# Kernel optimization log

Hardware: AMD Instinct MI355X
Metric: run time of the kernel (lower is better)

The kernel has to match this reference:

```python
import jax, jax.numpy as jnp
import numpy as np

H_HEADS = 32
KV_HEADS = 8
HEAD_DIM = 128
HIDDEN = 2048
EPS = 1e-6


def rms_norm(x, w):
    # normalize over last dim (head_dim)
    var = jnp.mean(jnp.square(x), axis=-1, keepdims=True)
    return x * jax.lax.rsqrt(var + EPS) * w


def rotate_half(x):
    x1, x2 = jnp.split(x, 2, axis=-1)
    return jnp.concatenate([-x2, x1], axis=-1)


def setup_inputs() -> dict:
    key = jax.random.key(0)
    ks = jax.random.split(key, 8)
    B, Q, CTX = 1, 1024, 2048
    T = CTX + Q
    hidden_states = jax.random.normal(ks[0], (B, Q, HIDDEN), jnp.float32)
    target_hidden = jax.random.normal(ks[1], (B, CTX, HIDDEN), jnp.float32)
    # RoPE tables over the full concatenated length
    inv_freq = 1.0 / (10000.0 ** (np.arange(0, HEAD_DIM, 2, dtype=np.float32) / HEAD_DIM))
    pos = np.arange(T, dtype=np.float32)
    freqs = np.outer(pos, inv_freq)                     # [T, hd/2]
    emb = np.concatenate([freqs, freqs], axis=-1)       # [T, hd]
    cos = jnp.asarray(np.cos(emb))[None]                # [1, T, hd]
    sin = jnp.asarray(np.sin(emb))[None]
    # custom mask: context fully visible, causal within noise block
    noise_causal = jnp.tril(jnp.ones((Q, Q), bool))
    mask = jnp.concatenate([jnp.ones((Q, CTX), bool), noise_causal], axis=1)
    attention_mask = mask[None, None]                   # [1,1,Q,T]
    scale = 0.02
    wq = jax.random.normal(ks[2], (H_HEADS * HEAD_DIM, HIDDEN), jnp.float32) * scale
    wk = jax.random.normal(ks[3], (KV_HEADS * HEAD_DIM, HIDDEN), jnp.float32) * scale
    wv = jax.random.normal(ks[4], (KV_HEADS * HEAD_DIM, HIDDEN), jnp.float32) * scale
    wo = jax.random.normal(ks[5], (HIDDEN, H_HEADS * HEAD_DIM), jnp.float32) * scale
    q_norm_w = jnp.ones((HEAD_DIM,), jnp.float32)
    k_norm_w = jnp.ones((HEAD_DIM,), jnp.float32)
    return {"hidden_states": hidden_states, "target_hidden": target_hidden,
            "cos": cos, "sin": sin, "attention_mask": attention_mask,
            "wq": wq, "wk": wk, "wv": wv, "wo": wo,
            "q_norm_w": q_norm_w, "k_norm_w": k_norm_w}


def reference(hidden_states, target_hidden, cos, sin, attention_mask,
              wq, wk, wv, wo, q_norm_w, k_norm_w):
    B, Q, _ = hidden_states.shape
    CTX = target_hidden.shape[1]
    T = CTX + Q
    n_rep = H_HEADS // KV_HEADS
    scaling = HEAD_DIM ** -0.5

    # Q from noise tokens, QK-RMSNorm per head
    q = (hidden_states @ wq.T).reshape(B, Q, H_HEADS, HEAD_DIM)
    q = rms_norm(q, q_norm_w).transpose(0, 2, 1, 3)          # [B,H,Q,hd]

    # K/V: context then noise, concatenated along sequence
    k = jnp.concatenate([target_hidden @ wk.T, hidden_states @ wk.T], axis=1)
    k = rms_norm(k.reshape(B, T, KV_HEADS, HEAD_DIM), k_norm_w).transpose(0, 2, 1, 3)  # [B,Hk,T,hd]
    v = jnp.concatenate([target_hidden @ wv.T, hidden_states @ wv.T], axis=1)
    v = v.reshape(B, T, KV_HEADS, HEAD_DIM).transpose(0, 2, 1, 3)                       # [B,Hk,T,hd]

    # offset RoPE: K uses all T positions, Q uses the last Q positions
    cos_b = cos[:, None]                                      # [B,1,T,hd]
    sin_b = sin[:, None]
    q = q * cos_b[:, :, -Q:, :] + rotate_half(q) * sin_b[:, :, -Q:, :]
    k = k * cos_b + rotate_half(k) * sin_b

    # GQA attention without materializing repeated K/V
    qg = q.reshape(B, KV_HEADS, n_rep, Q, HEAD_DIM)
    scores = jnp.einsum('bgrqd,bgtd->bgrqt', qg, k) * scaling  # [B,Hk,rep,Q,T]
    scores = jnp.where(attention_mask[:, :, None], scores, jnp.finfo(scores.dtype).min)
    probs = jax.nn.softmax(scores, axis=-1)
    out = jnp.einsum('bgrqt,bgtd->bgrqd', probs, v)            # [B,Hk,rep,Q,hd]
    out = out.reshape(B, H_HEADS, Q, HEAD_DIM).transpose(0, 2, 1, 3).reshape(B, Q, H_HEADS * HEAD_DIM)
    return out @ wo.T
```

## Files before the change

### kernel.cpp

```cpp
#include <hip/hip_runtime.h>

#define HIDDEN 2048
#define NQ     1024
#define NCTX   2048
#define NTOT   3072
#define NHEADS 32
#define KVH    8
#define HD     128

typedef __attribute__((ext_vector_type(8))) __bf16 bf16x8;
typedef __attribute__((ext_vector_type(4))) __bf16 bf16x4;
typedef __attribute__((ext_vector_type(4))) float  f32x4;

#define MFMA16(a, b, c) __builtin_amdgcn_mfma_f32_16x16x32_bf16(a, b, c, 0, 0, 0)

#define MSTATIC 12.0f

__device__ __forceinline__ void load_lds16(const void* g, void* l) {
    __builtin_amdgcn_global_load_lds(
        (const __attribute__((address_space(1))) unsigned int*)g,
        (__attribute__((address_space(3))) unsigned int*)l, 16, 0, 0);
}

__global__ __launch_bounds__(256) void conv2_f32_bf16(const float* __restrict__ s0,
                                                      __bf16* __restrict__ d0, int n0,
                                                      const float* __restrict__ s1,
                                                      __bf16* __restrict__ d1, int n1) {
    const float* s = blockIdx.y ? s1 : s0;
    __bf16*      d = blockIdx.y ? d1 : d0;
    int          n = blockIdx.y ? n1 : n0;
    int i = blockIdx.x * 256 + threadIdx.x;
    int stride = gridDim.x * 256;
    for (; i < n; i += stride) {
        float4 v = ((const float4*)s)[i];
        bf16x4 o;
        o[0] = (__bf16)v.x; o[1] = (__bf16)v.y;
        o[2] = (__bf16)v.z; o[3] = (__bf16)v.w;
        ((bf16x4*)d)[i] = o;
    }
}

template <typename OutT>
__device__ __forceinline__ void gemm128_f32b(const __bf16* __restrict__ Ablk,
                                             const float* __restrict__ Bblk,
                                             OutT* __restrict__ Cblk,
                                             int K, int lda, int ldb, int ldc) {
    __shared__ __bf16 As[128][64];
    __shared__ __bf16 Bs[128][64];

    const int tid  = threadIdx.x;
    const int lane = tid & 63;
    const int w    = tid >> 6;
    const int n16  = lane & 15;
    const int quad = lane >> 4;
    const int wm = (w & 1) * 64;
    const int wn = (w >> 1) * 64;

    f32x4 acc[4][4];
    const f32x4 fzero = {0.f, 0.f, 0.f, 0.f};
#pragma unroll
    for (int i = 0; i < 4; i++)
#pragma unroll
        for (int j = 0; j < 4; j++) acc[i][j] = fzero;

    const int srow = w * 32 + (lane >> 3);
    const int scol = (lane & 7) * 8;

    for (int k0 = 0; k0 < K; k0 += 64) {
#pragma unroll
        for (int i = 0; i < 4; i++) {
            int r = srow + i * 8;
            load_lds16(Ablk + (long)r * lda + k0 + scol, &As[r][scol]);
        }
#pragma unroll
        for (int i = 0; i < 4; i++) {
            int id = tid + i * 256;
            int br = id >> 3, c8 = (id & 7) * 8;
            float4 f0 = *(const float4*)(Bblk + (long)br * ldb + k0 + c8);
            float4 f1 = *(const float4*)(Bblk + (long)br * ldb + k0 + c8 + 4);
            bf16x8 bb;
            bb[0] = (__bf16)f0.x; bb[1] = (__bf16)f0.y;
            bb[2] = (__bf16)f0.z; bb[3] = (__bf16)f0.w;
            bb[4] = (__bf16)f1.x; bb[5] = (__bf16)f1.y;
            bb[6] = (__bf16)f1.z; bb[7] = (__bf16)f1.w;
            *(bf16x8*)&Bs[br][c8] = bb;
        }
        __syncthreads();
#pragma unroll
        for (int ks = 0; ks < 2; ks++) {
            bf16x8 af[4], bfr[4];
#pragma unroll
            for (int i = 0; i < 4; i++)
                af[i] = *(const bf16x8*)&As[wm + i * 16 + n16][ks * 32 + quad * 8];
#pragma unroll
            for (int j = 0; j < 4; j++)
                bfr[j] = *(const bf16x8*)&Bs[wn + j * 16 + n16][ks * 32 + quad * 8];
#pragma unroll
            for (int i = 0; i < 4; i++)
#pragma unroll
                for (int j = 0; j < 4; j++)
                    acc[i][j] = MFMA16(af[i], bfr[j], acc[i][j]);
        }
        __syncthreads();
    }

#pragma unroll
    for (int i = 0; i < 4; i++)
#pragma unroll
        for (int j = 0; j < 4; j++)
#pragma unroll
            for (int r = 0; r < 4; r++)
                Cblk[(long)(wm + i * 16 + quad * 4 + r) * ldc + wn + j * 16 + n16] =
                    (OutT)acc[i][j][r];
}

__global__ __launch_bounds__(256) void gemm_kvq(const __bf16* __restrict__ tgtb,
                                                const __bf16* __restrict__ hidb,
                                                const float* __restrict__ wk,
                                                const float* __restrict__ wv,
                                                const float* __restrict__ wq,
                                                __bf16* __restrict__ kbf,
                                                __bf16* __restrict__ vbf,
                                                __bf16* __restrict__ qbf) {
    const int b = blockIdx.x;
    const __bf16* Ap; const float* Bp; __bf16* Cp; int ldc;
    if (b < 384) {
        const int z = b / 192, bb = b - z * 192;
        const int n0 = (bb & 7) * 128, m0 = (bb >> 3) * 128;
        Ap = (m0 < 2048) ? tgtb + (long)m0 * 2048 : hidb + (long)(m0 - 2048) * 2048;
        Bp = (z ? wv : wk) + (long)n0 * 2048;
        Cp = (z ? vbf : kbf) + (long)m0 * 1024 + n0;
        ldc = 1024;
    } else {
        const int bb = b - 384;
        const int n0 = (bb & 31) * 128, m0 = (bb >> 5) * 128;
        Ap = hidb + (long)m0 * 2048;
        Bp = wq + (long)n0 * 2048;
        Cp = qbf + (long)m0 * 4096 + n0;
        ldc = 4096;
    }
    gemm128_f32b<__bf16>(Ap, Bp, Cp, 2048, 2048, 2048, ldc);
}

__global__ __launch_bounds__(256) void gemm_wo_splitk(const __bf16* __restrict__ A,
                                                      const float* __restrict__ B,
                                                      float* __restrict__ po) {
    const int m0 = blockIdx.y * 128;
    const int n0 = blockIdx.x * 128;
    const int koff = blockIdx.z * 1024;
    float* C = po + (long)blockIdx.z * 1024 * 2048;
    gemm128_f32b<float>(A + (long)m0 * 4096 + koff, B + (long)n0 * 4096 + koff,
                        C + (long)m0 * 2048 + n0, 1024, 4096, 4096, 2048);
}

__global__ __launch_bounds__(256) void add4(const float* __restrict__ po,
                                            float* __restrict__ out, int n4) {
    int i = blockIdx.x * 256 + threadIdx.x;
    int stride = gridDim.x * 256;
    const long seg = (long)1024 * 2048 / 4;
    for (; i < n4; i += stride) {
        float4 a = ((const float4*)po)[i];
        float4 b = ((const float4*)po)[i + seg];
        float4 c = ((const float4*)po)[i + 2 * seg];
        float4 d = ((const float4*)po)[i + 3 * seg];
        float4 o;
        o.x = (a.x + b.x) + (c.x + d.x);
        o.y = (a.y + b.y) + (c.y + d.y);
        o.z = (a.z + b.z) + (c.z + d.z);
        o.w = (a.w + b.w) + (c.w + d.w);
        ((float4*)out)[i] = o;
    }
}

__global__ __launch_bounds__(256) void rmsnorm_rope2(__bf16* __restrict__ xq,
                                                     const float* __restrict__ wq,
                                                     __bf16* __restrict__ xk,
                                                     const float* __restrict__ wk,
                                                     const float* __restrict__ cosb,
                                                     const float* __restrict__ sinb) {
    const int z = blockIdx.y;
    __bf16*      x = z ? xk : xq;
    const float* w = z ? wk : wq;
    const int nheads     = z ? 8 : 32;
    const int row_stride = z ? 1024 : 4096;
    const int pos_offset = z ? 0 : 2048;
    const float outscale = z ? 1.0f : 0.08838834764831845f;
    const int nitems     = z ? 3072 * 8 : 1024 * 32;

    int item = blockIdx.x * 4 + (threadIdx.x >> 6);
    int lane = threadIdx.x & 63;
    if (item >= nitems) return;
    int row = item / nheads;
    int head = item - row * nheads;
    __bf16* p = x + (long)row * row_stride + head * HD;

    float x1 = (float)p[lane], x2 = (float)p[lane + 64];
    float ss = x1 * x1 + x2 * x2;
#pragma unroll
    for (int o = 32; o >= 1; o >>= 1) ss += __shfl_xor(ss, o);
    float r = rsqrtf(ss * (1.0f / 128.0f) + 1e-6f) * outscale;

    int pos = pos_offset + row;
    float c1 = cosb[pos * HD + lane], c2 = cosb[pos * HD + lane + 64];
    float s1 = sinb[pos * HD + lane], s2 = sinb[pos * HD + lane + 64];
    float y1 = x1 * r * w[lane];
    float y2 = x2 * r * w[lane + 64];
    p[lane]      = (__bf16)(y1 * c1 - y2 * s1);
    p[lane + 64] = (__bf16)(y2 * c2 + y1 * s2);
}

__global__ __launch_bounds__(256) void transpose_v(const __bf16* __restrict__ v,
                                                   __bf16* __restrict__ vt) {
    __shared__ __bf16 T[64][68];
    const int tid = threadIdx.x;
    const int t0 = blockIdx.x * 64;
    const int d0 = blockIdx.y * 64;
    const int g  = blockIdx.z;
    const __bf16* src = v + (long)t0 * 1024 + g * 128 + d0;
#pragma unroll
    for (int i = 0; i < 4; i++) {
        int idx = tid + i * 256;
        int r = idx >> 4, c4 = (idx & 15) * 4;
        *(bf16x4*)&T[r][c4] = *(const bf16x4*)(src + (long)r * 1024 + c4);
    }
    __syncthreads();
    __bf16* dst = vt + (long)g * 128 * 3072 + (long)d0 * 3072 + t0;
#pragma unroll
    for (int i = 0; i < 4; i++) {
        int idx = tid + i * 256;
        int r = idx >> 4, c4 = (idx & 15) * 4;
        bf16x4 o;
        o[0] = T[c4 + 0][r]; o[1] = T[c4 + 1][r];
        o[2] = T[c4 + 2][r]; o[3] = T[c4 + 3][r];
        *(bf16x4*)(dst + (long)r * 3072 + c4) = o;
    }
}

__global__ __launch_bounds__(256) void flash_attn_splitk(const __bf16* __restrict__ qb,
                                                         const __bf16* __restrict__ kb,
                                                         const __bf16* __restrict__ vtg,
                                                         __bf16* __restrict__ Opart0,
                                                         __bf16* __restrict__ Opart1,
                                                         float* __restrict__ lsum) {
    __shared__ __bf16 KsU[64 * 136];
    __shared__ __bf16 Vs[128][72];
#define KS(r, c) KsU[(r) * 136 + (c)]
#define PS(w_, m_, t_) KsU[(w_) * 2176 + (m_) * 68 + (t_)]

    const int tid  = threadIdx.x;
    const int lane = tid & 63;
    const int w    = tid >> 6;
    const int n    = lane & 15;
    const int quad = lane >> 4;

    const int bid = blockIdx.x;
    const int s   = blockIdx.y;
    const int g  = bid & 7;
    const int jj = bid >> 3;
    const int h  = g * 4 + (jj & 3);
    const int qt = jj >> 2;

    const int qr0 = qt * 128 + w * 16;

    bf16x8 qf[2][4];
#pragma unroll
    for (int mt = 0; mt < 2; mt++) {
        const __bf16* qp = qb + (long)(qr0 + mt * 64 + n) * 4096 + h * 128 + quad * 8;
        qf[mt][0] = *(const bf16x8*)(qp);
        qf[mt][1] = *(const bf16x8*)(qp + 32);
        qf[mt][2] = *(const bf16x8*)(qp + 64);
        qf[mt][3] = *(const bf16x8*)(qp + 96);
    }

    f32x4 O[2][8];
    const f32x4 fzero = {0.f, 0.f, 0.f, 0.f};
#pragma unroll
    for (int mt = 0; mt < 2; mt++)
#pragma unroll
        for (int dt = 0; dt < 8; dt++) O[mt][dt] = fzero;
    float l_loc[2] = {0.f, 0.f};

    const int ntot = 34 + 2 * qt;
    const int half = ntot >> 1;
    const int tbeg = s ? half : 0;
    const int tend = s ? ntot : half;

    const int krr = tid >> 4, kc8 = (tid & 15) * 8;
    const int vrr = tid >> 3, vc8 = (tid & 7) * 8;
    const __bf16* kp = kb + g * 128 + (long)(tbeg * 64 + krr) * 1024 + kc8;
    const __bf16* vp = vtg + (long)g * 128 * 3072 + (long)vrr * 3072 + tbeg * 64 + vc8;

    for (int tt = tbeg; tt < tend; tt++) {
#pragma unroll
        for (int i = 0; i < 4; i++)
            *(bf16x8*)&KS(krr + i * 16, kc8) = *(const bf16x8*)(kp + (long)i * 16 * 1024);
#pragma unroll
        for (int i = 0; i < 4; i++)
            *(bf16x8*)&Vs[vrr + i * 32][vc8] = *(const bf16x8*)(vp + (long)i * 32 * 3072);
        kp += 64 * 1024;
        vp += 64;
        __syncthreads();

        f32x4 S[2][4];
#pragma unroll
        for (int nt = 0; nt < 4; nt++) {
            f32x4 a0 = fzero, a1 = fzero;
#pragma unroll
            for (int ks = 0; ks < 4; ks++) {
                bf16x8 kf = *(const bf16x8*)&KS(nt * 16 + n, ks * 32 + quad * 8);
                a0 = MFMA16(kf, qf[0][ks], a0);
                a1 = MFMA16(kf, qf[1][ks], a1);
            }
            S[0][nt] = a0;
            S[1][nt] = a1;
        }

        if (tt >= ntot - 2) {
            const int t0 = tt * 64;
#pragma unroll
            for (int mt = 0; mt < 2; mt++) {
                const int lim = 2048 + qr0 + mt * 64 + n;
#pragma unroll
                for (int nt = 0; nt < 4; nt++)
#pragma unroll
                    for (int r = 0; r < 4; r++) {
                        int t = t0 + nt * 16 + quad * 4 + r;
                        if (t > lim) S[mt][nt][r] = -1e30f;
                    }
            }
        }

        __syncthreads();

#pragma unroll
        for (int mt = 0; mt < 2; mt++)
#pragma unroll
            for (int nt = 0; nt < 4; nt++)
#pragma unroll
                for (int r = 0; r < 4; r++) {
                    float p = __expf(S[mt][nt][r] - MSTATIC);
                    S[mt][nt][r] = p;
                    l_loc[mt] += p;
                }

#pragma unroll
        for (int mt = 0; mt < 2; mt++)
#pragma unroll
            for (int nt = 0; nt < 4; nt++) {
                bf16x4 pk;
#pragma unroll
                for (int r = 0; r < 4; r++) pk[r] = (__bf16)S[mt][nt][r];
                *(bf16x4*)&PS(w, mt * 16 + n, nt * 16 + quad * 4) = pk;
            }

        bf16x8 pa[2][2];
#pragma unroll
        for (int mt = 0; mt < 2; mt++)
#pragma unroll
            for (int kg = 0; kg < 2; kg++)
                pa[mt][kg] = *(const bf16x8*)&PS(w, mt * 16 + n, kg * 32 + quad * 8);

#pragma unroll
        for (int dt = 0; dt < 8; dt++) {
            bf16x8 vf0 = *(const bf16x8*)&Vs[dt * 16 + n][quad * 8];
            bf16x8 vf1 = *(const bf16x8*)&Vs[dt * 16 + n][32 + quad * 8];
#pragma unroll
            for (int mt = 0; mt < 2; mt++) {
                f32x4 acc = O[mt][dt];
                acc = MFMA16(pa[mt][0], vf0, acc);
                acc = MFMA16(pa[mt][1], vf1, acc);
                O[mt][dt] = acc;
            }
        }
        __syncthreads();
    }

#pragma unroll
    for (int mt = 0; mt < 2; mt++) {
        float sm = l_loc[mt];
        sm += __shfl_xor(sm, 16);
        sm += __shfl_xor(sm, 32);
        l_loc[mt] = sm;
    }

    __bf16* Op = s ? Opart1 : Opart0;
    const long tb = (long)(h * 8 + qt) * 128 * 128;
#pragma unroll
    for (int mt = 0; mt < 2; mt++)
#pragma unroll
        for (int dt = 0; dt < 8; dt++)
#pragma unroll
            for (int r = 0; r < 4; r++)
                Op[tb + (long)(mt * 64 + w * 16 + quad * 4 + r) * 128 + dt * 16 + n] =
                    (__bf16)O[mt][dt][r];
    if (quad == 0) {
        const int lb = (s * 256 + h * 8 + qt) * 128 + w * 16;
#pragma unroll
        for (int mt = 0; mt < 2; mt++)
            lsum[lb + mt * 64 + n] = l_loc[mt];
    }
#undef KS
#undef PS
}

__global__ __launch_bounds__(256) void flash_merge(const __bf16* __restrict__ O0,
                                                   const __bf16* __restrict__ O1,
                                                   const float* __restrict__ lsum,
                                                   __bf16* __restrict__ ob) {
    const int bx = blockIdx.x;
    const int h   = bx >> 4;
    const int r6  = bx & 15;
    const int qt  = r6 >> 1;
    const int sub = r6 & 1;
    const int row  = threadIdx.x >> 2;
    const int cseg = (threadIdx.x & 3) * 32;
    const int mrow = sub * 64 + row;

    const int tilei = h * 8 + qt;
    float inv = 1.0f / (lsum[tilei * 128 + mrow] + lsum[(256 + tilei) * 128 + mrow]);

    const long src = (long)tilei * 128 * 128 + (long)mrow * 128 + cseg;
    __bf16* dst = ob + (long)(qt * 128 + mrow) * 4096 + h * 128 + cseg;
#pragma unroll
    for (int j = 0; j < 4; j++) {
        bf16x8 x0 = *(const bf16x8*)(O0 + src + j * 8);
        bf16x8 x1 = *(const bf16x8*)(O1 + src + j * 8);
        bf16x8 o;
#pragma unroll
        for (int k = 0; k < 8; k++)
            o[k] = (__bf16)(((float)x0[k] + (float)x1[k]) * inv);
        *(bf16x8*)(dst + j * 8) = o;
    }
}

extern "C" void kernel_launch(void* const* d_in, const int* in_sizes, int n_in,
                              void* d_out, int out_size, void* d_ws, size_t ws_size,
                              hipStream_t stream) {
    const float* hidden = (const float*)d_in[0];
    const float* target = (const float*)d_in[1];
    const float* cosb   = (const float*)d_in[2];
    const float* sinb   = (const float*)d_in[3];
    const float* wq = (const float*)d_in[5];
    const float* wk = (const float*)d_in[6];
    const float* wv = (const float*)d_in[7];
    const float* wo = (const float*)d_in[8];
    const float* qw = (const float*)d_in[9];
    const float* kw = (const float*)d_in[10];
    float* out = (float*)d_out;

    char* ws = (char*)d_ws;
    const long MB = 1 << 20;
    __bf16* qbf  = (__bf16*)(ws);
    __bf16* kbf  = (__bf16*)(ws + 8 * MB);
    __bf16* vbf  = (__bf16*)(ws + 14 * MB);
    __bf16* hidb = (__bf16*)(ws + 20 * MB);
    __bf16* tgtb = (__bf16*)(ws + 24 * MB);
    __bf16* vtg  = (__bf16*)(ws + 24 * MB);
    __bf16* Op1  = (__bf16*)(ws + 14 * MB);
    float*  lbuf = (float*)(ws + 22 * MB);
    __bf16* Op0  = (__bf16*)(ws + 30 * MB);
    float*  po   = (float*)(ws + 8 * MB);

    dim3 blk(256);

    conv2_f32_bf16<<<dim3(1024, 2), blk, 0, stream>>>(
        target, tgtb, (2048 * 2048) / 4, hidden, hidb, (1024 * 2048) / 4);

    gemm_kvq<<<640, blk, 0, stream>>>(tgtb, hidb, wk, wv, wq, kbf, vbf, qbf);

    rmsnorm_rope2<<<dim3(8192, 2), blk, 0, stream>>>(qbf, qw, kbf, kw, cosb, sinb);

    transpose_v<<<dim3(48, 2, 8), blk, 0, stream>>>(vbf, vtg);

    flash_attn_splitk<<<dim3(256, 2), blk, 0, stream>>>(qbf, kbf, vtg, Op0, Op1, lbuf);
    flash_merge<<<512, blk, 0, stream>>>(Op0, Op1, lbuf, qbf);

    gemm_wo_splitk<<<dim3(16, 8, 4), blk, 0, stream>>>(qbf, wo, po);
    add4<<<1024, blk, 0, stream>>>(po, out, (1024 * 2048) / 4);
}
```

Measured before the change: 393.0 us.

## Double-buffer LDS tiles and XOR-swizzle layout in projection GEMM

The shared GEMM helper now keeps two LDS buffers for A and B. It prefetches the next K-tile (A via async global-to-LDS loads, B via registers) while the MFMAs run on the current tile, which also drops one barrier per iteration. LDS columns are XOR-swizzled by row to reduce bank conflicts on the fragment reads. This doubles LDS use and adds register pressure for the prefetched B values, which may lower occupancy.

```diff
diff --git a/kernel.cpp b/kernel.cpp
--- a/kernel.cpp
+++ b/kernel.cpp
@@ -45,8 +45,8 @@
                                              const float* __restrict__ Bblk,
                                              OutT* __restrict__ Cblk,
                                              int K, int lda, int ldb, int ldc) {
-    __shared__ __bf16 As[128][64];
-    __shared__ __bf16 Bs[128][64];
+    __shared__ __bf16 As[2][128][64];
+    __shared__ __bf16 Bs[2][128][64];
 
     const int tid  = threadIdx.x;
     const int lane = tid & 63;
@@ -63,46 +63,80 @@
 #pragma unroll
         for (int j = 0; j < 4; j++) acc[i][j] = fzero;
 
-    const int srow = w * 32 + (lane >> 3);
-    const int scol = (lane & 7) * 8;
-
-    for (int k0 = 0; k0 < K; k0 += 64) {
-#pragma unroll
-        for (int i = 0; i < 4; i++) {
-            int r = srow + i * 8;
-            load_lds16(Ablk + (long)r * lda + k0 + scol, &As[r][scol]);
+    const int srow  = w * 32 + (lane >> 3);
+    const int sxor  = (lane >> 3) & 7;
+    const int scol  = (lane & 7) * 8;
+    const int sgcol = ((lane & 7) ^ sxor) * 8;
+    const __bf16* Aptr = Ablk + (long)srow * lda + sgcol;
+
+    const int br0  = tid >> 3;
+    const int bxor = br0 & 7;
+    const int bgc  = (tid & 7) * 8;
+    const int bwc  = ((tid & 7) ^ bxor) * 8;
+    const float* Bptr = Bblk + (long)br0 * ldb + bgc;
+
+    const int rx = n16 & 7;
+
+    float4 breg[4][2];
+
+#define STAGE_A(bi, kk)                                                        \
+    _Pragma("unroll") for (int i = 0; i < 4; i++)                              \
+        load_lds16(Aptr + (long)i * 8 * lda + (kk), &As[bi][srow + i * 8][scol]);
+
+#define LOAD_B(kk)                                                             \
+    _Pragma("unroll") for (int i = 0; i < 4; i++) {                            \
+        breg[i][0] = *(const float4*)(Bptr + (long)i * 32 * ldb + (kk));       \
+        breg[i][1] = *(const float4*)(Bptr + (long)i * 32 * ldb + (kk) + 4);   \
+    }
+
+#define WRITE_B(bi)                                                            \
+    _Pragma("unroll") for (int i = 0; i < 4; i++) {                            \
+        bf16x8 bb;                                                             \
+        bb[0] = (__bf16)breg[i][0].x; bb[1] = (__bf16)breg[i][0].y;            \
+        bb[2] = (__bf16)breg[i][0].z; bb[3] = (__bf16)breg[i][0].w;            \
+        bb[4] = (__bf16)breg[i][1].x; bb[5] = (__bf16)breg[i][1].y;            \
+        bb[6] = (__bf16)breg[i][1].z; bb[7] = (__bf16)breg[i][1].w;            \
+        *(bf16x8*)&Bs[bi][br0 + i * 32][bwc] = bb;                             \
+    }
+
+    STAGE_A(0, 0);
+    LOAD_B(0);
+    WRITE_B(0);
+    __syncthreads();
+
+    int buf = 0;
+    for (int k0 = 0;; k0 += 64) {
+        const bool last = (k0 + 64 >= K);
+        if (!last) {
+            STAGE_A(buf ^ 1, k0 + 64);
+            LOAD_B(k0 + 64);
         }
-#pragma unroll
-        for (int i = 0; i < 4; i++) {
-            int id = tid + i * 256;
-            int br = id >> 3, c8 = (id & 7) * 8;
-            float4 f0 = *(const float4*)(Bblk + (long)br * ldb + k0 + c8);
-            float4 f1 = *(const float4*)(Bblk + (long)br * ldb + k0 + c8 + 4);
-            bf16x8 bb;
-            bb[0] = (__bf16)f0.x; bb[1] = (__bf16)f0.y;
-            bb[2] = (__bf16)f0.z; bb[3] = (__bf16)f0.w;
-            bb[4] = (__bf16)f1.x; bb[5] = (__bf16)f1.y;
-            bb[6] = (__bf16)f1.z; bb[7] = (__bf16)f1.w;
-            *(bf16x8*)&Bs[br][c8] = bb;
-        }
-        __syncthreads();
 #pragma unroll
         for (int ks = 0; ks < 2; ks++) {
             bf16x8 af[4], bfr[4];
 #pragma unroll
             for (int i = 0; i < 4; i++)
-                af[i] = *(const bf16x8*)&As[wm + i * 16 + n16][ks * 32 + quad * 8];
+                af[i] = *(const bf16x8*)
+                    &As[buf][wm + i * 16 + n16][((ks * 4 + quad) ^ rx) * 8];
 #pragma unroll
             for (int j = 0; j < 4; j++)
-                bfr[j] = *(const bf16x8*)&Bs[wn + j * 16 + n16][ks * 32 + quad * 8];
+                bfr[j] = *(const bf16x8*)
+                    &Bs[buf][wn + j * 16 + n16][((ks * 4 + quad) ^ rx) * 8];
 #pragma unroll
             for (int i = 0; i < 4; i++)
 #pragma unroll
                 for (int j = 0; j < 4; j++)
                     acc[i][j] = MFMA16(af[i], bfr[j], acc[i][j]);
         }
+        if (last) break;
+        WRITE_B(buf ^ 1);
         __syncthreads();
-    }
+        buf ^= 1;
+    }
+
+#undef STAGE_A
+#undef LOAD_B
+#undef WRITE_B
 
 #pragma unroll
     for (int i = 0; i < 4; i++)
```

Result: faster. 376.1 us (-4.3%).

## Pre-convert weights to bf16, swizzle LDS, prefetch fp32 B tiles, halve Wo split-K

Applied to the files above, without the earlier changes.

Wk, Wv and Wo are now converted to bf16 once in bulk kernels, so the projection GEMMs can stream both operands straight into LDS with global_load_lds. LDS tiles use an XOR swizzle to avoid bank conflicts. The Q projection, which still reads fp32 weights, prefetches the next B tile into registers to overlap the load with compute. The output projection changes from split-K 4 to split-K 2, writing one partial directly into the output, with a smaller add pass afterwards. In exchange it adds extra conversion passes over the weights and reuses the workspace and output buffers more aggressively.

```diff
diff --git a/kernel.cpp b/kernel.cpp
--- a/kernel.cpp
+++ b/kernel.cpp
@@ -22,13 +22,21 @@
         (__attribute__((address_space(3))) unsigned int*)l, 16, 0, 0);
 }
 
-__global__ __launch_bounds__(256) void conv2_f32_bf16(const float* __restrict__ s0,
+__global__ __launch_bounds__(256) void conv4_f32_bf16(const float* __restrict__ s0,
                                                       __bf16* __restrict__ d0, int n0,
                                                       const float* __restrict__ s1,
-                                                      __bf16* __restrict__ d1, int n1) {
-    const float* s = blockIdx.y ? s1 : s0;
-    __bf16*      d = blockIdx.y ? d1 : d0;
-    int          n = blockIdx.y ? n1 : n0;
+                                                      __bf16* __restrict__ d1, int n1,
+                                                      const float* __restrict__ s2,
+                                                      __bf16* __restrict__ d2, int n2,
+                                                      const float* __restrict__ s3,
+                                                      __bf16* __restrict__ d3, int n3) {
+    const float* s; __bf16* d; int n;
+    switch (blockIdx.y) {
+        case 0:  s = s0; d = d0; n = n0; break;
+        case 1:  s = s1; d = d1; n = n1; break;
+        case 2:  s = s2; d = d2; n = n2; break;
+        default: s = s3; d = d3; n = n3; break;
+    }
     int i = blockIdx.x * 256 + threadIdx.x;
     int stride = gridDim.x * 256;
     for (; i < n; i += stride) {
@@ -40,14 +48,63 @@
     }
 }
 
+__global__ __launch_bounds__(256) void conv_wo(const float* __restrict__ wo,
+                                               __bf16* __restrict__ w0,
+                                               __bf16* __restrict__ w1) {
+    int i = blockIdx.x * 256 + threadIdx.x;
+    int stride = gridDim.x * 256;
+    for (; i < 2048 * 1024; i += stride) {
+        int r = i >> 10, cc = i & 1023;
+        float4 v = ((const float4*)wo)[i];
+        bf16x4 o;
+        o[0] = (__bf16)v.x; o[1] = (__bf16)v.y;
+        o[2] = (__bf16)v.z; o[3] = (__bf16)v.w;
+        __bf16* dst = (cc & 512) ? w1 : w0;
+        *(bf16x4*)(dst + (long)r * 2048 + (cc & 511) * 4) = o;
+    }
+}
+
+__device__ __forceinline__ void gemm_compute64(const __bf16 (&As)[128][64],
+                                               const __bf16 (&Bs)[128][64],
+                                               f32x4 (&acc)[4][4],
+                                               int wm, int wn, int n16, int quad, int rx) {
+#pragma unroll
+    for (int ks = 0; ks < 2; ks++) {
+        bf16x8 af[4], bfr[4];
+#pragma unroll
+        for (int i = 0; i < 4; i++)
+            af[i] = *(const bf16x8*)&As[wm + i * 16 + n16][((ks * 4 + quad) ^ rx) * 8];
+#pragma unroll
+        for (int j = 0; j < 4; j++)
+            bfr[j] = *(const bf16x8*)&Bs[wn + j * 16 + n16][((ks * 4 + quad) ^ rx) * 8];
+#pragma unroll
+        for (int i = 0; i < 4; i++)
+#pragma unroll
+            for (int j = 0; j < 4; j++)
+                acc[i][j] = MFMA16(af[i], bfr[j], acc[i][j]);
+    }
+}
+
 template <typename OutT>
-__device__ __forceinline__ void gemm128_f32b(const __bf16* __restrict__ Ablk,
-                                             const float* __restrict__ Bblk,
-                                             OutT* __restrict__ Cblk,
-                                             int K, int lda, int ldb, int ldc) {
-    __shared__ __bf16 As[128][64];
-    __shared__ __bf16 Bs[128][64];
-
+__device__ __forceinline__ void gemm_epilogue(const f32x4 (&acc)[4][4],
+                                              OutT* __restrict__ Cblk, int ldc,
+                                              int wm, int wn, int n16, int quad) {
+#pragma unroll
+    for (int i = 0; i < 4; i++)
+#pragma unroll
+        for (int j = 0; j < 4; j++)
+#pragma unroll
+            for (int r = 0; r < 4; r++)
+                Cblk[(long)(wm + i * 16 + quad * 4 + r) * ldc + wn + j * 16 + n16] =
+                    (OutT)acc[i][j][r];
+}
+
+template <typename OutT>
+__device__ __forceinline__ void gemm128_bb(__bf16 (&As)[128][64], __bf16 (&Bs)[128][64],
+                                           const __bf16* __restrict__ Ablk,
+                                           const __bf16* __restrict__ Bblk,
+                                           OutT* __restrict__ Cblk,
+                                           int K, int lda, int ldb, int ldc) {
     const int tid  = threadIdx.x;
     const int lane = tid & 63;
     const int w    = tid >> 6;
@@ -63,111 +120,145 @@
 #pragma unroll
         for (int j = 0; j < 4; j++) acc[i][j] = fzero;
 
-    const int srow = w * 32 + (lane >> 3);
-    const int scol = (lane & 7) * 8;
+    const int srow  = w * 32 + (lane >> 3);
+    const int sxor  = (lane >> 3) & 7;
+    const int scol  = (lane & 7) * 8;
+    const int sgcol = ((lane & 7) ^ sxor) * 8;
+    const __bf16* Ap = Ablk + (long)srow * lda + sgcol;
+    const __bf16* Bp = Bblk + (long)srow * ldb + sgcol;
+    const int rx = n16 & 7;
 
     for (int k0 = 0; k0 < K; k0 += 64) {
 #pragma unroll
         for (int i = 0; i < 4; i++) {
-            int r = srow + i * 8;
-            load_lds16(Ablk + (long)r * lda + k0 + scol, &As[r][scol]);
+            load_lds16(Ap + (long)i * 8 * lda + k0, &As[srow + i * 8][scol]);
+            load_lds16(Bp + (long)i * 8 * ldb + k0, &Bs[srow + i * 8][scol]);
         }
+        __syncthreads();
+        gemm_compute64(As, Bs, acc, wm, wn, n16, quad, rx);
+        __syncthreads();
+    }
+    gemm_epilogue(acc, Cblk, ldc, wm, wn, n16, quad);
+}
+
+template <typename OutT>
+__device__ __forceinline__ void gemm128_fb(__bf16 (&As)[128][64], __bf16 (&Bs)[128][64],
+                                           const __bf16* __restrict__ Ablk,
+                                           const float* __restrict__ Bblk,
+                                           OutT* __restrict__ Cblk,
+                                           int K, int lda, int ldb, int ldc) {
+    const int tid  = threadIdx.x;
+    const int lane = tid & 63;
+    const int w    = tid >> 6;
+    const int n16  = lane & 15;
+    const int quad = lane >> 4;
+    const int wm = (w & 1) * 64;
+    const int wn = (w >> 1) * 64;
+
+    f32x4 acc[4][4];
+    const f32x4 fzero = {0.f, 0.f, 0.f, 0.f};
+#pragma unroll
+    for (int i = 0; i < 4; i++)
+#pragma unroll
+        for (int j = 0; j < 4; j++) acc[i][j] = fzero;
+
+    const int srow  = w * 32 + (lane >> 3);
+    const int sxor  = (lane >> 3) & 7;
+    const int scol  = (lane & 7) * 8;
+    const int sgcol = ((lane & 7) ^ sxor) * 8;
+    const __bf16* Ap = Ablk + (long)srow * lda + sgcol;
+
+    const int br0  = tid >> 3;
+    const int bxor = br0 & 7;
+    const int bgc  = (tid & 7) * 8;
+    const int bwc  = ((tid & 7) ^ bxor) * 8;
+    const float* Bptr = Bblk + (long)br0 * ldb + bgc;
+
+    const int rx = n16 & 7;
+    float4 breg[4][2];
+
+#define LOAD_B(kk)                                                             \
+    _Pragma("unroll") for (int i = 0; i < 4; i++) {                            \
+        breg[i][0] = *(const float4*)(Bptr + (long)i * 32 * ldb + (kk));       \
+        breg[i][1] = *(const float4*)(Bptr + (long)i * 32 * ldb + (kk) + 4);   \
+    }
+
+    LOAD_B(0);
+    for (int k0 = 0; k0 < K; k0 += 64) {
+#pragma unroll
+        for (int i = 0; i < 4; i++)
+            load_lds16(Ap + (long)i * 8 * lda + k0, &As[srow + i * 8][scol]);
 #pragma unroll
         for (int i = 0; i < 4; i++) {
-            int id = tid + i * 256;
-            int br = id >> 3, c8 = (id & 7) * 8;
-            float4 f0 = *(const float4*)(Bblk + (long)br * ldb + k0 + c8);
-            float4 f1 = *(const float4*)(Bblk + (long)br * ldb + k0 + c8 + 4);
             bf16x8 bb;
-            bb[0] = (__bf16)f0.x; bb[1] = (__bf16)f0.y;
-            bb[2] = (__bf16)f0.z; bb[3] = (__bf16)f0.w;
-            bb[4] = (__bf16)f1.x; bb[5] = (__bf16)f1.y;
-            bb[6] = (__bf16)f1.z; bb[7] = (__bf16)f1.w;
-            *(bf16x8*)&Bs[br][c8] = bb;
+            bb[0] = (__bf16)breg[i][0].x; bb[1] = (__bf16)breg[i][0].y;
+            bb[2] = (__bf16)breg[i][0].z; bb[3] = (__bf16)breg[i][0].w;
+            bb[4] = (__bf16)breg[i][1].x; bb[5] = (__bf16)breg[i][1].y;
+            bb[6] = (__bf16)breg[i][1].z; bb[7] = (__bf16)breg[i][1].w;
+            *(bf16x8*)&Bs[br0 + i * 32][bwc] = bb;
         }
-        __syncthreads();
-#pragma unroll
-        for (int ks = 0; ks < 2; ks++) {
-            bf16x8 af[4], bfr[4];
-#pragma unroll
-            for (int i = 0; i < 4; i++)
-                af[i] = *(const bf16x8*)&As[wm + i * 16 + n16][ks * 32 + quad * 8];
-#pragma unroll
-            for (int j = 0; j < 4; j++)
-                bfr[j] = *(const bf16x8*)&Bs[wn + j * 16 + n16][ks * 32 + quad * 8];
-#pragma unroll
-            for (int i = 0; i < 4; i++)
-#pragma unroll
-                for (int j = 0; j < 4; j++)
-                    acc[i][j] = MFMA16(af[i], bfr[j], acc[i][j]);
-        }
-        __syncthreads();
-    }
-
-#pragma unroll
-    for (int i = 0; i < 4; i++)
-#pragma unroll
-        for (int j = 0; j < 4; j++)
-#pragma unroll
-            for (int r = 0; r < 4; r++)
-                Cblk[(long)(wm + i * 16 + quad * 4 + r) * ldc + wn + j * 16 + n16] =
-                    (OutT)acc[i][j][r];
+        if (k0 + 64 < K) LOAD_B(k0 + 64);
+        __syncthreads();
+        gemm_compute64(As, Bs, acc, wm, wn, n16, quad, rx);
+        __syncthreads();
+    }
+#undef LOAD_B
+    gemm_epilogue(acc, Cblk, ldc, wm, wn, n16, quad);
 }
 
 __global__ __launch_bounds__(256) void gemm_kvq(const __bf16* __restrict__ tgtb,
                                                 const __bf16* __restrict__ hidb,
-                                                const float* __restrict__ wk,
-                                                const float* __restrict__ wv,
+                                                const __bf16* __restrict__ wkb,
+                                                const __bf16* __restrict__ wvb,
                                                 const float* __restrict__ wq,
                                                 __bf16* __restrict__ kbf,
                                                 __bf16* __restrict__ vbf,
                                                 __bf16* __restrict__ qbf) {
+    __shared__ __bf16 As[128][64];
+    __shared__ __bf16 Bs[128][64];
     const int b = blockIdx.x;
-    const __bf16* Ap; const float* Bp; __bf16* Cp; int ldc;
     if (b < 384) {
         const int z = b / 192, bb = b - z * 192;
         const int n0 = (bb & 7) * 128, m0 = (bb >> 3) * 128;
-        Ap = (m0 < 2048) ? tgtb + (long)m0 * 2048 : hidb + (long)(m0 - 2048) * 2048;
-        Bp = (z ? wv : wk) + (long)n0 * 2048;
-        Cp = (z ? vbf : kbf) + (long)m0 * 1024 + n0;
-        ldc = 1024;
+        const __bf16* Ap = (m0 < 2048) ? tgtb + (long)m0 * 2048
+                                       : hidb + (long)(m0 - 2048) * 2048;
+        const __bf16* Bp = (z ? wvb : wkb) + (long)n0 * 2048;
+        __bf16* Cp = (z ? vbf : kbf) + (long)m0 * 1024 + n0;
+        gemm128_bb<__bf16>(As, Bs, Ap, Bp, Cp, 2048, 2048, 2048, 1024);
     } else {
         const int bb = b - 384;
         const int n0 = (bb & 31) * 128, m0 = (bb >> 5) * 128;
-        Ap = hidb + (long)m0 * 2048;
-        Bp = wq + (long)n0 * 2048;
-        Cp = qbf + (long)m0 * 4096 + n0;
-        ldc = 4096;
-    }
-    gemm128_f32b<__bf16>(Ap, Bp, Cp, 2048, 2048, 2048, ldc);
-}
-
-__global__ __launch_bounds__(256) void gemm_wo_splitk(const __bf16* __restrict__ A,
-                                                      const float* __restrict__ B,
-                                                      float* __restrict__ po) {
+        gemm128_fb<__bf16>(As, Bs, hidb + (long)m0 * 2048, wq + (long)n0 * 2048,
+                           qbf + (long)m0 * 4096 + n0, 2048, 2048, 2048, 4096);
+    }
+}
+
+__global__ __launch_bounds__(256) void gemm_wo2(const __bf16* __restrict__ A,
+                                                const __bf16* __restrict__ w0,
+                                                const __bf16* __restrict__ w1,
+                                                float* __restrict__ out,
+                                                float* __restrict__ po1) {
+    __shared__ __bf16 As[128][64];
+    __shared__ __bf16 Bs[128][64];
     const int m0 = blockIdx.y * 128;
     const int n0 = blockIdx.x * 128;
-    const int koff = blockIdx.z * 1024;
-    float* C = po + (long)blockIdx.z * 1024 * 2048;
-    gemm128_f32b<float>(A + (long)m0 * 4096 + koff, B + (long)n0 * 4096 + koff,
-                        C + (long)m0 * 2048 + n0, 1024, 4096, 4096, 2048);
-}
-
-__global__ __launch_bounds__(256) void add4(const float* __restrict__ po,
-                                            float* __restrict__ out, int n4) {
+    const int z  = blockIdx.z;
+    const __bf16* Bp = (z ? w1 : w0) + (long)n0 * 2048;
+    float* C = (z ? po1 : out) + (long)m0 * 2048 + n0;
+    gemm128_bb<float>(As, Bs, A + (long)m0 * 4096 + z * 2048, Bp, C,
+                      2048, 4096, 2048, 2048);
+}
+
+__global__ __launch_bounds__(256) void add2_inplace(float* __restrict__ out,
+                                                    const float* __restrict__ p1, int n4) {
     int i = blockIdx.x * 256 + threadIdx.x;
     int stride = gridDim.x * 256;
-    const long seg = (long)1024 * 2048 / 4;
     for (; i < n4; i += stride) {
-        float4 a = ((const float4*)po)[i];
-        float4 b = ((const float4*)po)[i + seg];
-        float4 c = ((const float4*)po)[i + 2 * seg];
-        float4 d = ((const float4*)po)[i + 3 * seg];
+        float4 a = ((const float4*)out)[i];
+        float4 b = ((const float4*)p1)[i];
         float4 o;
-        o.x = (a.x + b.x) + (c.x + d.x);
-        o.y = (a.y + b.y) + (c.y + d.y);
-        o.z = (a.z + b.z) + (c.z + d.z);
-        o.w = (a.w + b.w) + (c.w + d.w);
+        o.x = a.x + b.x; o.y = a.y + b.y;
+        o.z = a.z + b.z; o.w = a.w + b.w;
         ((float4*)out)[i] = o;
     }
 }
@@ -450,31 +541,38 @@
 
     char* ws = (char*)d_ws;
     const long MB = 1 << 20;
-    __bf16* qbf  = (__bf16*)(ws);
-    __bf16* kbf  = (__bf16*)(ws + 8 * MB);
-    __bf16* vbf  = (__bf16*)(ws + 14 * MB);
-    __bf16* hidb = (__bf16*)(ws + 20 * MB);
-    __bf16* tgtb = (__bf16*)(ws + 24 * MB);
-    __bf16* vtg  = (__bf16*)(ws + 24 * MB);
-    __bf16* Op1  = (__bf16*)(ws + 14 * MB);
-    float*  lbuf = (float*)(ws + 22 * MB);
-    __bf16* Op0  = (__bf16*)(ws + 30 * MB);
-    float*  po   = (float*)(ws + 8 * MB);
+    __bf16* hidb = (__bf16*)(ws);
+    __bf16* tgtb = (__bf16*)(ws + 4 * MB);
+    __bf16* wkb  = (__bf16*)(ws + 12 * MB);
+    __bf16* wvb  = (__bf16*)(ws + 16 * MB);
+    __bf16* kbf  = (__bf16*)(ws + 20 * MB);
+    __bf16* vbf  = (__bf16*)(ws + 26 * MB);
+    __bf16* vtg  = (__bf16*)(ws + 32 * MB);
+    float*  lbuf = (float*)(ws);
+    __bf16* Op0  = (__bf16*)(ws + 4 * MB);
+    __bf16* Op1  = (__bf16*)(ws + 12 * MB);
+    __bf16* attnb= (__bf16*)(ws + 20 * MB);
+    __bf16* wob0 = (__bf16*)(ws + 4 * MB);
+    __bf16* wob1 = (__bf16*)(ws + 12 * MB);
+    float*  po1  = (float*)(ws + 28 * MB);
+    __bf16* qbf  = (__bf16*)d_out;
 
     dim3 blk(256);
 
-    conv2_f32_bf16<<<dim3(1024, 2), blk, 0, stream>>>(
-        target, tgtb, (2048 * 2048) / 4, hidden, hidb, (1024 * 2048) / 4);
-
-    gemm_kvq<<<640, blk, 0, stream>>>(tgtb, hidb, wk, wv, wq, kbf, vbf, qbf);
+    conv4_f32_bf16<<<dim3(1024, 4), blk, 0, stream>>>(
+        hidden, hidb, (1024 * 2048) / 4, target, tgtb, (2048 * 2048) / 4,
+        wk, wkb, (1024 * 2048) / 4, wv, wvb, (1024 * 2048) / 4);
+
+    gemm_kvq<<<640, blk, 0, stream>>>(tgtb, hidb, wkb, wvb, wq, kbf, vbf, qbf);
 
     rmsnorm_rope2<<<dim3(8192, 2), blk, 0, stream>>>(qbf, qw, kbf, kw, cosb, sinb);
 
     transpose_v<<<dim3(48, 2, 8), blk, 0, stream>>>(vbf, vtg);
 
     flash_attn_splitk<<<dim3(256, 2), blk, 0, stream>>>(qbf, kbf, vtg, Op0, Op1, lbuf);
-    flash_merge<<<512, blk, 0, stream>>>(Op0, Op1, lbuf, qbf);
-
-    gemm_wo_splitk<<<dim3(16, 8, 4), blk, 0, stream>>>(qbf, wo, po);
-    add4<<<1024, blk, 0, stream>>>(po, out, (1024 * 2048) / 4);
-}
+    flash_merge<<<512, blk, 0, stream>>>(Op0, Op1, lbuf, attnb);
+
+    conv_wo<<<2048, blk, 0, stream>>>(wo, wob0, wob1);
+    gemm_wo2<<<dim3(16, 8, 2), blk, 0, stream>>>(attnb, wob0, wob1, out, po1);
+    add2_inplace<<<1024, blk, 0, stream>>>(out, po1, (1024 * 2048) / 4);
+}
```

After: 360.0 us. -8.4%, faster.
